# Performance work log

Hardware: AMD Instinct MI355X
Metric: run time of the kernel (lower is better)

## Reference

```python
import math
import jax, jax.numpy as jnp
import numpy as np

B, T, C, H = 1, 2048, 1024, 16


def _rope(q, k):
    # q, k: (B, H, T, D); interleaved RoPE exactly as the torch helper
    D = q.shape[-1]
    pos = jnp.arange(q.shape[2], dtype=jnp.float32)[:, None]           # (T, 1)
    div = jnp.exp(jnp.arange(0, D, 2, dtype=jnp.float32) * (-math.log(10000.0) / D))
    ang = pos * div                                                     # (T, D/2)
    sin = jnp.repeat(jnp.sin(ang), 2, axis=-1)                          # [s0,s0,s1,s1,...]
    cos = jnp.repeat(jnp.cos(ang), 2, axis=-1)

    def rot(x):
        x_alt = jnp.stack([-x[..., 1::2], x[..., ::2]], axis=-1).reshape(x.shape)
        return x * cos + x_alt * sin

    return rot(q), rot(k)


def setup_inputs() -> dict:
    key = jax.random.key(0)
    ks = jax.random.split(key, 5)
    s = 1.0 / math.sqrt(C)
    return {
        "x": jax.random.normal(ks[0], (B, T, C), dtype=jnp.float32),
        "Wq": jax.random.normal(ks[1], (C, C), dtype=jnp.float32) * s,
        "bq": jnp.zeros((C,), dtype=jnp.float32),
        "Wk": jax.random.normal(ks[2], (C, C), dtype=jnp.float32) * s,
        "bk": jnp.zeros((C,), dtype=jnp.float32),
        "Wv": jax.random.normal(ks[3], (C, C), dtype=jnp.float32) * s,
        "bv": jnp.zeros((C,), dtype=jnp.float32),
        "Wp": jax.random.normal(ks[4], (C, C), dtype=jnp.float32) * s,
        "bp": jnp.zeros((C,), dtype=jnp.float32),
    }


def reference(x, Wq, bq, Wk, bk, Wv, bv, Wp, bp):
    b, t, c = x.shape
    d = c // H
    # QKV projections -> (B, H, T, D)
    def split_heads(y):
        return y.reshape(b, t, H, d).transpose(0, 2, 1, 3)

    q = split_heads(x @ Wq + bq)
    k = split_heads(x @ Wk + bk)
    v = split_heads(x @ Wv + bv)
    q, k = _rope(q, k)

    scale = 1.0 / math.sqrt(d)
    att = jnp.einsum("bhqd,bhkd->bhqk", q, k) * scale                   # (B,H,T,T)
    causal = jnp.tril(jnp.ones((t, t), dtype=bool))                     # (T,T)
    att = jnp.where(causal[None, None], att, -jnp.inf)
    att = jax.nn.softmax(att, axis=-1)
    attn_save = att
    # dropout p=0 (eval) -> identity
    y = jnp.einsum("bhqk,bhkd->bhqd", att, v)                           # (B,H,T,D)
    y = y.transpose(0, 2, 1, 3).reshape(b, t, c)
    y = y @ Wp + bp
    return y, attn_save
```

## Files before the change

kernel.cpp:

```cpp
#include <hip/hip_runtime.h>

typedef unsigned short ushort_t;
typedef __bf16 bf16x8 __attribute__((ext_vector_type(8)));
typedef float f32x4 __attribute__((ext_vector_type(4)));

#define T_DIM 2048
#define C_DIM 1024
#define H_NUM 16
#define D_DIM 64

__device__ __forceinline__ ushort_t f2bf(float f){
  unsigned v = __float_as_uint(f);
  return (ushort_t)((v + 0x7fffu + ((v >> 16) & 1u)) >> 16);
}
__device__ __forceinline__ float bf2f(ushort_t u){
  return __uint_as_float(((unsigned)u) << 16);
}

typedef __attribute__((address_space(1))) const unsigned int* gas1_t;
typedef __attribute__((address_space(3))) unsigned int* las3_t;

__device__ __forceinline__ void gload_lds16(const void* g, void* l){
  __builtin_amdgcn_global_load_lds((gas1_t)g, (las3_t)l, 16, 0, 0);
}

__global__ __launch_bounds__(256) void prep_kernel(
    const float* __restrict__ x, ushort_t* __restrict__ xb,
    const float* __restrict__ w0, const float* __restrict__ w1,
    const float* __restrict__ w2, const float* __restrict__ w3,
    ushort_t* __restrict__ t0, ushort_t* __restrict__ t1,
    ushort_t* __restrict__ t2, ushort_t* __restrict__ t3)
{
  __shared__ float tl[64][65];
  const int bid = blockIdx.x;
  const int tid = threadIdx.x;
  if (bid >= 1024){
    int i = ((bid - 1024) * 256 + tid) * 4;
    float4 v = *reinterpret_cast<const float4*>(x + i);
    ushort4 o;
    o.x = f2bf(v.x); o.y = f2bf(v.y); o.z = f2bf(v.z); o.w = f2bf(v.w);
    *reinterpret_cast<ushort4*>(xb + i) = o;
    return;
  }
  const int which = bid >> 8;
  const float* W = which==0 ? w0 : which==1 ? w1 : which==2 ? w2 : w3;
  ushort_t* WT   = which==0 ? t0 : which==1 ? t1 : which==2 ? t2 : t3;
  const int tile = bid & 255;
  const int k0 = (tile & 15) * 64;
  const int n0 = (tile >> 4) * 64;
#pragma unroll
  for (int i = 0; i < 16; ++i){
    int idx = tid + i * 256;
    int r = idx >> 6, c = idx & 63;
    tl[r][c] = W[(k0 + r) * C_DIM + n0 + c];
  }
  __syncthreads();
#pragma unroll
  for (int i = 0; i < 16; ++i){
    int idx = tid + i * 256;
    int r = idx >> 6, c = idx & 63;
    WT[(n0 + r) * C_DIM + k0 + c] = f2bf(tl[c][r]);
  }
}

template<int MODE>
__global__ __launch_bounds__(256) void gemm_kernel(
    const ushort_t* __restrict__ A,
    const ushort_t* __restrict__ bt0, const ushort_t* __restrict__ bt1, const ushort_t* __restrict__ bt2,
    const float* __restrict__ bias0, const float* __restrict__ bias1, const float* __restrict__ bias2,
    ushort_t* __restrict__ o0, ushort_t* __restrict__ o1, ushort_t* __restrict__ o2,
    float* __restrict__ fo)
{
  __shared__ __align__(16) ushort_t Alds[64 * 32];
  __shared__ __align__(16) ushort_t Blds[128 * 32];
  const int tid = threadIdx.x;
  const int l15 = tid & 15, g = (tid & 63) >> 4;
  const int w = tid >> 6, wr = w >> 1, wc = w & 1;
  const int m0 = blockIdx.x * 64;
  int byy = blockIdx.y;
  int sel = 0;
  const ushort_t* BT; const float* bias; ushort_t* outp;
  if (MODE == 0){
    sel = byy >> 3; byy &= 7;
    BT   = sel==0 ? bt0 : (sel==1 ? bt1 : bt2);
    bias = sel==0 ? bias0 : (sel==1 ? bias1 : bias2);
    outp = sel==0 ? o0 : (sel==1 ? o1 : o2);
  } else { BT = bt0; bias = bias0; outp = o0; }
  const int n0 = byy * 128;

  const int c0 = tid, c1 = tid + 256;
  const ushort_t* Asrc  = A + (m0 + (c0 >> 2)) * C_DIM + (c0 & 3) * 8;
  const ushort_t* Bsrc0 = BT + (n0 + (c0 >> 2)) * C_DIM + (c0 & 3) * 8;
  const ushort_t* Bsrc1 = BT + (n0 + (c1 >> 2)) * C_DIM + (c1 & 3) * 8;

  f32x4 acc[2][4] = {};

  for (int kt = 0; kt < 32; ++kt){
    const int ko = kt * 32;
    gload_lds16(Asrc + ko, &Alds[c0 * 8]);
    gload_lds16(Bsrc0 + ko, &Blds[c0 * 8]);
    gload_lds16(Bsrc1 + ko, &Blds[c1 * 8]);
    __syncthreads();
    bf16x8 af[2], bfr[4];
#pragma unroll
    for (int i = 0; i < 2; ++i)
      af[i] = *reinterpret_cast<const bf16x8*>(&Alds[(wr * 32 + i * 16 + l15) * 32 + g * 8]);
#pragma unroll
    for (int j = 0; j < 4; ++j)
      bfr[j] = *reinterpret_cast<const bf16x8*>(&Blds[(wc * 64 + j * 16 + l15) * 32 + g * 8]);
#pragma unroll
    for (int i = 0; i < 2; ++i)
#pragma unroll
      for (int j = 0; j < 4; ++j)
        acc[i][j] = __builtin_amdgcn_mfma_f32_16x16x32_bf16(af[i], bfr[j], acc[i][j], 0, 0, 0);
    __syncthreads();
  }

  float bvv[4];
#pragma unroll
  for (int j = 0; j < 4; ++j) bvv[j] = bias[n0 + wc * 64 + j * 16 + l15];

  if (MODE == 1){
#pragma unroll
    for (int i = 0; i < 2; ++i)
#pragma unroll
      for (int j = 0; j < 4; ++j)
#pragma unroll
        for (int e = 0; e < 4; ++e){
          int t = m0 + wr * 32 + i * 16 + g * 4 + e;
          int c = n0 + wc * 64 + j * 16 + l15;
          fo[t * C_DIM + c] = acc[i][j][e] + bvv[j];
        }
    return;
  }

  if (sel == 2){
#pragma unroll
    for (int i = 0; i < 2; ++i){
#pragma unroll
      for (int j = 0; j < 4; ++j){
        int c = n0 + wc * 64 + j * 16 + l15;
        int hh = c >> 6, d = c & 63;
        int t0e = m0 + wr * 32 + i * 16 + g * 4;
        ushort4 o;
        o.x = f2bf(acc[i][j][0] + bvv[j]);
        o.y = f2bf(acc[i][j][1] + bvv[j]);
        o.z = f2bf(acc[i][j][2] + bvv[j]);
        o.w = f2bf(acc[i][j][3] + bvv[j]);
        *reinterpret_cast<ushort4*>(outp + (size_t)(hh * D_DIM + d) * T_DIM + t0e) = o;
      }
    }
  } else {
#pragma unroll
    for (int i = 0; i < 2; ++i){
#pragma unroll
      for (int j = 0; j < 4; ++j){
#pragma unroll
        for (int e = 0; e < 4; ++e){
          int t = m0 + wr * 32 + i * 16 + g * 4 + e;
          int c = n0 + wc * 64 + j * 16 + l15;
          int hh = c >> 6, d = c & 63;
          outp[((size_t)(hh * T_DIM) + t) * D_DIM + d] = f2bf(acc[i][j][e] + bvv[j]);
        }
      }
    }
  }
}

__global__ void rope_kernel(ushort_t* __restrict__ Qb, ushort_t* __restrict__ Kb){
  int gid = blockIdx.x * 256 + threadIdx.x;
  int which = gid >> 20;
  int r = gid & ((1 << 20) - 1);
  int i = r & 31;
  int t = (r >> 5) & 2047;
  int hh = r >> 16;
  ushort_t* P = which ? Kb : Qb;
  unsigned* p = reinterpret_cast<unsigned*>(P + ((hh * T_DIM) + t) * D_DIM + 2 * i);
  unsigned pv = *p;
  float x0 = bf2f((ushort_t)(pv & 0xffffu));
  float x1 = bf2f((ushort_t)(pv >> 16));
  float ang = (float)t * __expf((float)i * -0.2878231366242558f);
  float sn, cs;
  __sincosf(ang, &sn, &cs);
  float y0 = x0 * cs - x1 * sn;
  float y1 = x1 * cs + x0 * sn;
  *p = (unsigned)f2bf(y0) | (((unsigned)f2bf(y1)) << 16);
}

__global__ __launch_bounds__(256) void attn_kernel(
    const ushort_t* __restrict__ Qb, const ushort_t* __restrict__ Kb,
    const ushort_t* __restrict__ Vt, float* __restrict__ att, ushort_t* __restrict__ ya)
{
  __shared__ __align__(16) ushort_t Plds[2][64 * 72];
  __shared__ float m_sh[64], l_sh[64];

  const int tid = threadIdx.x;
  const int l15 = tid & 15, g = (tid & 63) >> 4;
  const int w = tid >> 6, wr = w >> 1, wc = w & 1;
  const int lin = (int)blockIdx.x;
  const int h = 2 * (lin & 7) + ((lin >> 3) & 1);
  const int qi = (T_DIM / 64 - 1) - (lin >> 4);
  const int q0 = qi * 64;
  const int nkt = qi + 1;

  const ushort_t* Qh = Qb + h * T_DIM * D_DIM;
  const ushort_t* Kh = Kb + h * T_DIM * D_DIM;
  const ushort_t* Vh = Vt + h * D_DIM * T_DIM;
  float* atth = att + (size_t)h * T_DIM * T_DIM;

  const f32x4 fz = {0.f, 0.f, 0.f, 0.f};
  const float scale = 0.125f;

  const int qloc = w * 16 + l15;
  const int qglob = q0 + qloc;
  bf16x8 qT[2];
#pragma unroll
  for (int ks = 0; ks < 2; ++ks)
    qT[ks] = *reinterpret_cast<const bf16x8*>(Qh + qglob * D_DIM + ks * 32 + g * 8);

  float m1 = -1e30f, l1 = 0.f;

  for (int kt = 0; kt < nkt; ++kt){
    f32x4 sc[4];
    sc[0] = fz; sc[1] = fz; sc[2] = fz; sc[3] = fz;
#pragma unroll
    for (int mblk = 0; mblk < 4; ++mblk){
#pragma unroll
      for (int ks = 0; ks < 2; ++ks){
        bf16x8 kfT = *reinterpret_cast<const bf16x8*>(
            Kh + (kt * 64 + mblk * 16 + l15) * D_DIM + ks * 32 + g * 8);
        sc[mblk] = __builtin_amdgcn_mfma_f32_16x16x32_bf16(kfT, qT[ks], sc[mblk], 0, 0, 0);
      }
    }
    const bool diag = (kt == qi);
    const int kbase = kt * 64 + g * 4;
    float sv[16];
    float mx = -1e30f;
#pragma unroll
    for (int mblk = 0; mblk < 4; ++mblk){
#pragma unroll
      for (int j = 0; j < 4; ++j){
        float s = sc[mblk][j] * scale;
        if (diag && (kbase + mblk * 16 + j) > qglob) s = -1e30f;
        sv[mblk * 4 + j] = s;
        mx = fmaxf(mx, s);
      }
    }
    mx = fmaxf(mx, __shfl_xor(mx, 16));
    mx = fmaxf(mx, __shfl_xor(mx, 32));
    float mn = fmaxf(m1, mx);
    float ps = 0.f;
#pragma unroll
    for (int i = 0; i < 16; ++i) ps += __expf(sv[i] - mn);
    ps += __shfl_xor(ps, 16);
    ps += __shfl_xor(ps, 32);
    l1 = l1 * __expf(m1 - mn) + ps;
    m1 = mn;
  }

  if ((tid & 48) == 0){ m_sh[qloc] = m1; l_sh[qloc] = l1; }
  __syncthreads();

  float Mrow[2][4], Li[2][4];
#pragma unroll
  for (int ms = 0; ms < 2; ++ms)
#pragma unroll
    for (int j = 0; j < 4; ++j){
      int row = wr * 32 + ms * 16 + g * 4 + j;
      Mrow[ms][j] = m_sh[row];
      Li[ms][j] = 1.0f / l_sh[row];
    }

  bf16x8 qf[2][2];
#pragma unroll
  for (int ms = 0; ms < 2; ++ms)
#pragma unroll
    for (int ks = 0; ks < 2; ++ks)
      qf[ms][ks] = *reinterpret_cast<const bf16x8*>(
          Qh + (q0 + wr * 32 + ms * 16 + l15) * D_DIM + ks * 32 + g * 8);

  f32x4 yac[2][2];
  yac[0][0] = fz; yac[0][1] = fz; yac[1][0] = fz; yac[1][1] = fz;

  int pb = 0;
  for (int kt = 0; kt < nkt; ++kt){
    ushort_t* Pb = &Plds[pb][0];
    bf16x8 kf[2][2];
#pragma unroll
    for (int ns = 0; ns < 2; ++ns)
#pragma unroll
      for (int ks = 0; ks < 2; ++ks)
        kf[ns][ks] = *reinterpret_cast<const bf16x8*>(
            Kh + (kt * 64 + wc * 32 + ns * 16 + l15) * D_DIM + ks * 32 + g * 8);

    f32x4 sac[2][2];
    sac[0][0] = fz; sac[0][1] = fz; sac[1][0] = fz; sac[1][1] = fz;
#pragma unroll
    for (int ms = 0; ms < 2; ++ms)
#pragma unroll
      for (int ns = 0; ns < 2; ++ns)
#pragma unroll
        for (int ks = 0; ks < 2; ++ks)
          sac[ms][ns] = __builtin_amdgcn_mfma_f32_16x16x32_bf16(qf[ms][ks], kf[ns][ks], sac[ms][ns], 0, 0, 0);

    const bool diag = (kt == qi);
#pragma unroll
    for (int ms = 0; ms < 2; ++ms)
#pragma unroll
      for (int ns = 0; ns < 2; ++ns)
#pragma unroll
        for (int j = 0; j < 4; ++j){
          float s = sac[ms][ns][j] * scale;
          int qq = wr * 32 + ms * 16 + g * 4 + j;
          int cc = wc * 32 + ns * 16 + l15;
          if (diag && cc > qq) s = -1e30f;
          float p = __expf(s - Mrow[ms][j]) * Li[ms][j];
          Pb[qq * 72 + cc] = f2bf(p);
        }
    __syncthreads();

    bf16x8 pf[2][2], vf[2][2];
#pragma unroll
    for (int ms = 0; ms < 2; ++ms)
#pragma unroll
      for (int kk = 0; kk < 2; ++kk)
        pf[ms][kk] = *reinterpret_cast<const bf16x8*>(
            &Pb[(wr * 32 + ms * 16 + l15) * 72 + kk * 32 + g * 8]);
#pragma unroll
    for (int nd = 0; nd < 2; ++nd)
#pragma unroll
      for (int kk = 0; kk < 2; ++kk)
        vf[nd][kk] = *reinterpret_cast<const bf16x8*>(
            Vh + (wc * 32 + nd * 16 + l15) * T_DIM + kt * 64 + kk * 32 + g * 8);
#pragma unroll
    for (int ms = 0; ms < 2; ++ms)
#pragma unroll
      for (int nd = 0; nd < 2; ++nd)
#pragma unroll
        for (int kk = 0; kk < 2; ++kk)
          yac[ms][nd] = __builtin_amdgcn_mfma_f32_16x16x32_bf16(pf[ms][kk], vf[nd][kk], yac[ms][nd], 0, 0, 0);

#pragma unroll
    for (int half = 0; half < 2; ++half){
      const int c = tid + half * 256;
      const int r = c >> 3, s = c & 7;
      union { int4 i4; ushort_t us[8]; } u;
      u.i4 = *reinterpret_cast<const int4*>(&Pb[r * 72 + s * 8]);
      f32x4 lo = { bf2f(u.us[0]), bf2f(u.us[1]), bf2f(u.us[2]), bf2f(u.us[3]) };
      f32x4 hi = { bf2f(u.us[4]), bf2f(u.us[5]), bf2f(u.us[6]), bf2f(u.us[7]) };
      float* dst = atth + (size_t)(q0 + r) * T_DIM + kt * 64 + s * 8;
      __builtin_nontemporal_store(lo, reinterpret_cast<f32x4*>(dst));
      __builtin_nontemporal_store(hi, reinterpret_cast<f32x4*>(dst) + 1);
    }
    pb ^= 1;
  }

  const int zc0 = nkt * 64;
  const int cpr = (T_DIM - zc0) >> 2;
  if (cpr > 0){
    const f32x4 z = {0.f, 0.f, 0.f, 0.f};
    for (int r = 0; r < 64; ++r){
      f32x4* dst = reinterpret_cast<f32x4*>(atth + (size_t)(q0 + r) * T_DIM + zc0);
      for (int i = tid; i < cpr; i += 256)
        __builtin_nontemporal_store(z, dst + i);
    }
  }

#pragma unroll
  for (int ms = 0; ms < 2; ++ms)
#pragma unroll
    for (int nd = 0; nd < 2; ++nd)
#pragma unroll
      for (int j = 0; j < 4; ++j){
        int t = q0 + wr * 32 + ms * 16 + g * 4 + j;
        int dcol = wc * 32 + nd * 16 + l15;
        ya[t * C_DIM + h * D_DIM + dcol] = f2bf(yac[ms][nd][j]);
      }
}

extern "C" void kernel_launch(void* const* d_in, const int* in_sizes, int n_in,
                              void* d_out, int out_size, void* d_ws, size_t ws_size,
                              hipStream_t stream)
{
  const float* x  = (const float*)d_in[0];
  const float* Wq = (const float*)d_in[1];
  const float* bq = (const float*)d_in[2];
  const float* Wk = (const float*)d_in[3];
  const float* bk = (const float*)d_in[4];
  const float* Wv = (const float*)d_in[5];
  const float* bv = (const float*)d_in[6];
  const float* Wp = (const float*)d_in[7];
  const float* bp = (const float*)d_in[8];
  float* out = (float*)d_out;
  char* ws = (char*)d_ws;

  ushort_t* xb  = (ushort_t*)(ws);
  ushort_t* wtq = (ushort_t*)(ws + (4u  << 20));
  ushort_t* wtk = (ushort_t*)(ws + (6u  << 20));
  ushort_t* wtv = (ushort_t*)(ws + (8u  << 20));
  ushort_t* wtp = (ushort_t*)(ws + (10u << 20));
  ushort_t* Qb  = (ushort_t*)(ws + (12u << 20));
  ushort_t* Kb  = (ushort_t*)(ws + (16u << 20));
  ushort_t* Vt  = (ushort_t*)(ws + (20u << 20));
  ushort_t* ya  = (ushort_t*)(ws + (24u << 20));

  hipLaunchKernelGGL(prep_kernel, dim3(3072), dim3(256), 0, stream,
                     x, xb, Wq, Wk, Wv, Wp, wtq, wtk, wtv, wtp);
  hipLaunchKernelGGL((gemm_kernel<0>), dim3(32, 24), dim3(256), 0, stream,
                     xb, wtq, wtk, wtv, bq, bk, bv, Qb, Kb, Vt, nullptr);
  hipLaunchKernelGGL(rope_kernel, dim3(8192), dim3(256), 0, stream, Qb, Kb);
  hipLaunchKernelGGL(attn_kernel, dim3(512), dim3(256), 0, stream,
                     Qb, Kb, Vt, out + 2097152, ya);
  hipLaunchKernelGGL((gemm_kernel<1>), dim3(32, 8), dim3(256), 0, stream,
                     ya, wtp, nullptr, nullptr, bp, nullptr, nullptr,
                     nullptr, nullptr, nullptr, out);
}
```

Measured before the change: 181.1 us.

## Split attention along key tiles into two halves with stats merge and reduction

```diff
diff --git a/kernel.cpp b/kernel.cpp
--- a/kernel.cpp
+++ b/kernel.cpp
@@ -187,21 +187,103 @@
   *p = (unsigned)f2bf(y0) | (((unsigned)f2bf(y1)) << 16);
 }
 
-__global__ __launch_bounds__(256) void attn_kernel(
+__global__ __launch_bounds__(256) void attn_pass1_kernel(
     const ushort_t* __restrict__ Qb, const ushort_t* __restrict__ Kb,
-    const ushort_t* __restrict__ Vt, float* __restrict__ att, ushort_t* __restrict__ ya)
+    float* __restrict__ mS, float* __restrict__ lS)
+{
+  const int tid = threadIdx.x;
+  const int l15 = tid & 15, g = (tid & 63) >> 4;
+  const int w = tid >> 6;
+  const int lin = (int)blockIdx.x;
+  const int h = 2 * (lin & 7) + ((lin >> 3) & 1);
+  const int rest = lin >> 4;
+  const int qi = 31 - (rest >> 1);
+  const int s = rest & 1;
+  const int q0 = qi * 64;
+  const int nkt = qi + 1;
+  const int n1 = (nkt + 1) >> 1;
+  const int kt0 = s ? n1 : 0;
+  const int kt1 = s ? nkt : n1;
+
+  const ushort_t* Qh = Qb + h * T_DIM * D_DIM;
+  const ushort_t* Kh = Kb + h * T_DIM * D_DIM;
+  const f32x4 fz = {0.f, 0.f, 0.f, 0.f};
+  const float scale = 0.125f;
+
+  const int qloc = w * 16 + l15;
+  const int qglob = q0 + qloc;
+  bf16x8 qT[2];
+#pragma unroll
+  for (int ks = 0; ks < 2; ++ks)
+    qT[ks] = *reinterpret_cast<const bf16x8*>(Qh + qglob * D_DIM + ks * 32 + g * 8);
+
+  float m1 = -1e30f, l1 = 0.f;
+
+  for (int kt = kt0; kt < kt1; ++kt){
+    f32x4 sc[4];
+    sc[0] = fz; sc[1] = fz; sc[2] = fz; sc[3] = fz;
+#pragma unroll
+    for (int mblk = 0; mblk < 4; ++mblk){
+#pragma unroll
+      for (int ks = 0; ks < 2; ++ks){
+        bf16x8 kfT = *reinterpret_cast<const bf16x8*>(
+            Kh + (kt * 64 + mblk * 16 + l15) * D_DIM + ks * 32 + g * 8);
+        sc[mblk] = __builtin_amdgcn_mfma_f32_16x16x32_bf16(kfT, qT[ks], sc[mblk], 0, 0, 0);
+      }
+    }
+    const bool diag = (kt == qi);
+    const int kbase = kt * 64 + g * 4;
+    float sv[16];
+    float mx = -1e30f;
+#pragma unroll
+    for (int mblk = 0; mblk < 4; ++mblk){
+#pragma unroll
+      for (int j = 0; j < 4; ++j){
+        float sx = sc[mblk][j] * scale;
+        if (diag && (kbase + mblk * 16 + j) > qglob) sx = -1e30f;
+        sv[mblk * 4 + j] = sx;
+        mx = fmaxf(mx, sx);
+      }
+    }
+    mx = fmaxf(mx, __shfl_xor(mx, 16));
+    mx = fmaxf(mx, __shfl_xor(mx, 32));
+    float mn = fmaxf(m1, mx);
+    float ps = 0.f;
+#pragma unroll
+    for (int i = 0; i < 16; ++i) ps += __expf(sv[i] - mn);
+    ps += __shfl_xor(ps, 16);
+    ps += __shfl_xor(ps, 32);
+    l1 = l1 * __expf(m1 - mn) + ps;
+    m1 = mn;
+  }
+
+  if ((tid & 48) == 0){
+    mS[(h * 2 + s) * T_DIM + qglob] = m1;
+    lS[(h * 2 + s) * T_DIM + qglob] = l1;
+  }
+}
+
+__global__ __launch_bounds__(256) void attn_pass2_kernel(
+    const ushort_t* __restrict__ Qb, const ushort_t* __restrict__ Kb,
+    const ushort_t* __restrict__ Vt,
+    const float* __restrict__ mS, const float* __restrict__ lS,
+    float* __restrict__ att, float* __restrict__ yp)
 {
   __shared__ __align__(16) ushort_t Plds[2][64 * 72];
-  __shared__ float m_sh[64], l_sh[64];
 
   const int tid = threadIdx.x;
   const int l15 = tid & 15, g = (tid & 63) >> 4;
   const int w = tid >> 6, wr = w >> 1, wc = w & 1;
   const int lin = (int)blockIdx.x;
   const int h = 2 * (lin & 7) + ((lin >> 3) & 1);
-  const int qi = (T_DIM / 64 - 1) - (lin >> 4);
+  const int rest = lin >> 4;
+  const int qi = 31 - (rest >> 1);
+  const int s = rest & 1;
   const int q0 = qi * 64;
   const int nkt = qi + 1;
+  const int n1 = (nkt + 1) >> 1;
+  const int kt0 = s ? n1 : 0;
+  const int kt1 = s ? nkt : n1;
 
   const ushort_t* Qh = Qb + h * T_DIM * D_DIM;
   const ushort_t* Kh = Kb + h * T_DIM * D_DIM;
@@ -211,64 +293,20 @@
   const f32x4 fz = {0.f, 0.f, 0.f, 0.f};
   const float scale = 0.125f;
 
-  const int qloc = w * 16 + l15;
-  const int qglob = q0 + qloc;
-  bf16x8 qT[2];
-#pragma unroll
-  for (int ks = 0; ks < 2; ++ks)
-    qT[ks] = *reinterpret_cast<const bf16x8*>(Qh + qglob * D_DIM + ks * 32 + g * 8);
-
-  float m1 = -1e30f, l1 = 0.f;
-
-  for (int kt = 0; kt < nkt; ++kt){
-    f32x4 sc[4];
-    sc[0] = fz; sc[1] = fz; sc[2] = fz; sc[3] = fz;
-#pragma unroll
-    for (int mblk = 0; mblk < 4; ++mblk){
-#pragma unroll
-      for (int ks = 0; ks < 2; ++ks){
-        bf16x8 kfT = *reinterpret_cast<const bf16x8*>(
-            Kh + (kt * 64 + mblk * 16 + l15) * D_DIM + ks * 32 + g * 8);
-        sc[mblk] = __builtin_amdgcn_mfma_f32_16x16x32_bf16(kfT, qT[ks], sc[mblk], 0, 0, 0);
-      }
-    }
-    const bool diag = (kt == qi);
-    const int kbase = kt * 64 + g * 4;
-    float sv[16];
-    float mx = -1e30f;
-#pragma unroll
-    for (int mblk = 0; mblk < 4; ++mblk){
-#pragma unroll
-      for (int j = 0; j < 4; ++j){
-        float s = sc[mblk][j] * scale;
-        if (diag && (kbase + mblk * 16 + j) > qglob) s = -1e30f;
-        sv[mblk * 4 + j] = s;
-        mx = fmaxf(mx, s);
-      }
-    }
-    mx = fmaxf(mx, __shfl_xor(mx, 16));
-    mx = fmaxf(mx, __shfl_xor(mx, 32));
-    float mn = fmaxf(m1, mx);
-    float ps = 0.f;
-#pragma unroll
-    for (int i = 0; i < 16; ++i) ps += __expf(sv[i] - mn);
-    ps += __shfl_xor(ps, 16);
-    ps += __shfl_xor(ps, 32);
-    l1 = l1 * __expf(m1 - mn) + ps;
-    m1 = mn;
-  }
-
-  if ((tid & 48) == 0){ m_sh[qloc] = m1; l_sh[qloc] = l1; }
-  __syncthreads();
-
   float Mrow[2][4], Li[2][4];
 #pragma unroll
   for (int ms = 0; ms < 2; ++ms)
 #pragma unroll
     for (int j = 0; j < 4; ++j){
-      int row = wr * 32 + ms * 16 + g * 4 + j;
-      Mrow[ms][j] = m_sh[row];
-      Li[ms][j] = 1.0f / l_sh[row];
+      int row = q0 + wr * 32 + ms * 16 + g * 4 + j;
+      float ma = mS[(h * 2 + 0) * T_DIM + row];
+      float mb = mS[(h * 2 + 1) * T_DIM + row];
+      float la = lS[(h * 2 + 0) * T_DIM + row];
+      float lb = lS[(h * 2 + 1) * T_DIM + row];
+      float M = fmaxf(ma, mb);
+      float L = la * __expf(ma - M) + lb * __expf(mb - M);
+      Mrow[ms][j] = M;
+      Li[ms][j] = 1.0f / L;
     }
 
   bf16x8 qf[2][2];
@@ -283,7 +321,7 @@
   yac[0][0] = fz; yac[0][1] = fz; yac[1][0] = fz; yac[1][1] = fz;
 
   int pb = 0;
-  for (int kt = 0; kt < nkt; ++kt){
+  for (int kt = kt0; kt < kt1; ++kt){
     ushort_t* Pb = &Plds[pb][0];
     bf16x8 kf[2][2];
 #pragma unroll
@@ -310,11 +348,11 @@
       for (int ns = 0; ns < 2; ++ns)
 #pragma unroll
         for (int j = 0; j < 4; ++j){
-          float s = sac[ms][ns][j] * scale;
+          float sx = sac[ms][ns][j] * scale;
           int qq = wr * 32 + ms * 16 + g * 4 + j;
           int cc = wc * 32 + ns * 16 + l15;
-          if (diag && cc > qq) s = -1e30f;
-          float p = __expf(s - Mrow[ms][j]) * Li[ms][j];
+          if (diag && cc > qq) sx = -1e30f;
+          float p = __expf(sx - Mrow[ms][j]) * Li[ms][j];
           Pb[qq * 72 + cc] = f2bf(p);
         }
     __syncthreads();
@@ -343,29 +381,32 @@
 #pragma unroll
     for (int half = 0; half < 2; ++half){
       const int c = tid + half * 256;
-      const int r = c >> 3, s = c & 7;
+      const int r = c >> 3, sx = c & 7;
       union { int4 i4; ushort_t us[8]; } u;
-      u.i4 = *reinterpret_cast<const int4*>(&Pb[r * 72 + s * 8]);
+      u.i4 = *reinterpret_cast<const int4*>(&Pb[r * 72 + sx * 8]);
       f32x4 lo = { bf2f(u.us[0]), bf2f(u.us[1]), bf2f(u.us[2]), bf2f(u.us[3]) };
       f32x4 hi = { bf2f(u.us[4]), bf2f(u.us[5]), bf2f(u.us[6]), bf2f(u.us[7]) };
-      float* dst = atth + (size_t)(q0 + r) * T_DIM + kt * 64 + s * 8;
+      float* dst = atth + (size_t)(q0 + r) * T_DIM + kt * 64 + sx * 8;
       __builtin_nontemporal_store(lo, reinterpret_cast<f32x4*>(dst));
       __builtin_nontemporal_store(hi, reinterpret_cast<f32x4*>(dst) + 1);
     }
     pb ^= 1;
   }
 
-  const int zc0 = nkt * 64;
-  const int cpr = (T_DIM - zc0) >> 2;
-  if (cpr > 0){
-    const f32x4 z = {0.f, 0.f, 0.f, 0.f};
-    for (int r = 0; r < 64; ++r){
-      f32x4* dst = reinterpret_cast<f32x4*>(atth + (size_t)(q0 + r) * T_DIM + zc0);
-      for (int i = tid; i < cpr; i += 256)
-        __builtin_nontemporal_store(z, dst + i);
-    }
-  }
-
+  if (s == 1){
+    const int zc0 = nkt * 64;
+    const int cpr = (T_DIM - zc0) >> 2;
+    if (cpr > 0){
+      const f32x4 z = {0.f, 0.f, 0.f, 0.f};
+      for (int r = 0; r < 64; ++r){
+        f32x4* dst = reinterpret_cast<f32x4*>(atth + (size_t)(q0 + r) * T_DIM + zc0);
+        for (int i = tid; i < cpr; i += 256)
+          __builtin_nontemporal_store(z, dst + i);
+      }
+    }
+  }
+
+  float* ypd = yp + (size_t)s * (T_DIM * C_DIM);
 #pragma unroll
   for (int ms = 0; ms < 2; ++ms)
 #pragma unroll
@@ -374,8 +415,21 @@
       for (int j = 0; j < 4; ++j){
         int t = q0 + wr * 32 + ms * 16 + g * 4 + j;
         int dcol = wc * 32 + nd * 16 + l15;
-        ya[t * C_DIM + h * D_DIM + dcol] = f2bf(yac[ms][nd][j]);
-      }
+        ypd[(size_t)t * C_DIM + h * D_DIM + dcol] = yac[ms][nd][j];
+      }
+}
+
+__global__ void y_reduce_kernel(const float* __restrict__ yp, ushort_t* __restrict__ ya)
+{
+  int i = (blockIdx.x * 256 + threadIdx.x) * 4;
+  float4 a = *reinterpret_cast<const float4*>(yp + i);
+  float4 b = *reinterpret_cast<const float4*>(yp + (T_DIM * C_DIM) + i);
+  ushort4 o;
+  o.x = f2bf(a.x + b.x);
+  o.y = f2bf(a.y + b.y);
+  o.z = f2bf(a.z + b.z);
+  o.w = f2bf(a.w + b.w);
+  *reinterpret_cast<ushort4*>(ya + i) = o;
 }
 
 extern "C" void kernel_launch(void* const* d_in, const int* in_sizes, int n_in,
@@ -403,14 +457,20 @@
   ushort_t* Kb  = (ushort_t*)(ws + (16u << 20));
   ushort_t* Vt  = (ushort_t*)(ws + (20u << 20));
   ushort_t* ya  = (ushort_t*)(ws + (24u << 20));
+  float*    mS  = (float*)   (ws + (28u << 20));
+  float*    lS  = (float*)   (ws + (28u << 20) + (256u << 10));
+  float*    yp  = (float*)   (ws + (29u << 20));
 
   hipLaunchKernelGGL(prep_kernel, dim3(3072), dim3(256), 0, stream,
                      x, xb, Wq, Wk, Wv, Wp, wtq, wtk, wtv, wtp);
   hipLaunchKernelGGL((gemm_kernel<0>), dim3(32, 24), dim3(256), 0, stream,
                      xb, wtq, wtk, wtv, bq, bk, bv, Qb, Kb, Vt, nullptr);
   hipLaunchKernelGGL(rope_kernel, dim3(8192), dim3(256), 0, stream, Qb, Kb);
-  hipLaunchKernelGGL(attn_kernel, dim3(512), dim3(256), 0, stream,
-                     Qb, Kb, Vt, out + 2097152, ya);
+  hipLaunchKernelGGL(attn_pass1_kernel, dim3(1024), dim3(256), 0, stream,
+                     Qb, Kb, mS, lS);
+  hipLaunchKernelGGL(attn_pass2_kernel, dim3(1024), dim3(256), 0, stream,
+                     Qb, Kb, Vt, mS, lS, out + 2097152, yp);
+  hipLaunchKernelGGL(y_reduce_kernel, dim3(2048), dim3(256), 0, stream, yp, ya);
   hipLaunchKernelGGL((gemm_kernel<1>), dim3(32, 8), dim3(256), 0, stream,
                      ya, wtp, nullptr, nullptr, bp, nullptr, nullptr,
                      nullptr, nullptr, nullptr, out);
```

Result: slower. 220.1 us (+21.6%).

## Halve attention query block to 32 rows and split stats pass across key halves

Applied to the files above, without the earlier changes.

```diff
diff --git a/kernel.cpp b/kernel.cpp
--- a/kernel.cpp
+++ b/kernel.cpp
@@ -8,6 +8,7 @@
 #define C_DIM 1024
 #define H_NUM 16
 #define D_DIM 64
+#define QBLK 32
 
 __device__ __forceinline__ ushort_t f2bf(float f){
   unsigned v = __float_as_uint(f);
@@ -191,17 +192,19 @@
     const ushort_t* __restrict__ Qb, const ushort_t* __restrict__ Kb,
     const ushort_t* __restrict__ Vt, float* __restrict__ att, ushort_t* __restrict__ ya)
 {
-  __shared__ __align__(16) ushort_t Plds[2][64 * 72];
-  __shared__ float m_sh[64], l_sh[64];
+  __shared__ __align__(16) ushort_t Plds[2][QBLK * 72];
+  __shared__ float m_sh[2][QBLK], l_sh[2][QBLK];
 
   const int tid = threadIdx.x;
   const int l15 = tid & 15, g = (tid & 63) >> 4;
-  const int w = tid >> 6, wr = w >> 1, wc = w & 1;
+  const int w = tid >> 6;
   const int lin = (int)blockIdx.x;
   const int h = 2 * (lin & 7) + ((lin >> 3) & 1);
-  const int qi = (T_DIM / 64 - 1) - (lin >> 4);
-  const int q0 = qi * 64;
-  const int nkt = qi + 1;
+  const int qi = 63 - (lin >> 4);
+  const int q0 = qi * QBLK;
+  const int nkt = (qi >> 1) + 1;
+  const int kd = nkt - 1;
+  const int qoff = (qi & 1) * 32;
 
   const ushort_t* Qh = Qb + h * T_DIM * D_DIM;
   const ushort_t* Kh = Kb + h * T_DIM * D_DIM;
@@ -211,8 +214,9 @@
   const f32x4 fz = {0.f, 0.f, 0.f, 0.f};
   const float scale = 0.125f;
 
-  const int qloc = w * 16 + l15;
-  const int qglob = q0 + qloc;
+  const int qsel = w & 1, khalf = w >> 1;
+  const int lq = qsel * 16 + l15;
+  const int qglob = q0 + lq;
   bf16x8 qT[2];
 #pragma unroll
   for (int ks = 0; ks < 2; ++ks)
@@ -220,7 +224,7 @@
 
   float m1 = -1e30f, l1 = 0.f;
 
-  for (int kt = 0; kt < nkt; ++kt){
+  for (int kt = khalf; kt < nkt; kt += 2){
     f32x4 sc[4];
     sc[0] = fz; sc[1] = fz; sc[2] = fz; sc[3] = fz;
 #pragma unroll
@@ -232,8 +236,7 @@
         sc[mblk] = __builtin_amdgcn_mfma_f32_16x16x32_bf16(kfT, qT[ks], sc[mblk], 0, 0, 0);
       }
     }
-    const bool diag = (kt == qi);
-    const int kbase = kt * 64 + g * 4;
+    const bool diag = (kt == kd);
     float sv[16];
     float mx = -1e30f;
 #pragma unroll
@@ -241,7 +244,7 @@
 #pragma unroll
       for (int j = 0; j < 4; ++j){
         float s = sc[mblk][j] * scale;
-        if (diag && (kbase + mblk * 16 + j) > qglob) s = -1e30f;
+        if (diag && (mblk * 16 + g * 4 + j) > (qoff + lq)) s = -1e30f;
         sv[mblk * 4 + j] = s;
         mx = fmaxf(mx, s);
       }
@@ -258,29 +261,29 @@
     m1 = mn;
   }
 
-  if ((tid & 48) == 0){ m_sh[qloc] = m1; l_sh[qloc] = l1; }
+  if (g == 0){ m_sh[khalf][lq] = m1; l_sh[khalf][lq] = l1; }
   __syncthreads();
 
-  float Mrow[2][4], Li[2][4];
-#pragma unroll
-  for (int ms = 0; ms < 2; ++ms)
-#pragma unroll
-    for (int j = 0; j < 4; ++j){
-      int row = wr * 32 + ms * 16 + g * 4 + j;
-      Mrow[ms][j] = m_sh[row];
-      Li[ms][j] = 1.0f / l_sh[row];
-    }
-
-  bf16x8 qf[2][2];
-#pragma unroll
-  for (int ms = 0; ms < 2; ++ms)
-#pragma unroll
-    for (int ks = 0; ks < 2; ++ks)
-      qf[ms][ks] = *reinterpret_cast<const bf16x8*>(
-          Qh + (q0 + wr * 32 + ms * 16 + l15) * D_DIM + ks * 32 + g * 8);
-
-  f32x4 yac[2][2];
-  yac[0][0] = fz; yac[0][1] = fz; yac[1][0] = fz; yac[1][1] = fz;
+  const int wr = w >> 1, wc = w & 1;
+  float Mrow[4], Li[4];
+#pragma unroll
+  for (int j = 0; j < 4; ++j){
+    int row = wr * 16 + g * 4 + j;
+    float ma = m_sh[0][row], mb = m_sh[1][row];
+    float M = fmaxf(ma, mb);
+    float L = l_sh[0][row] * __expf(ma - M) + l_sh[1][row] * __expf(mb - M);
+    Mrow[j] = M;
+    Li[j] = 1.0f / L;
+  }
+
+  bf16x8 qf[2];
+#pragma unroll
+  for (int ks = 0; ks < 2; ++ks)
+    qf[ks] = *reinterpret_cast<const bf16x8*>(
+        Qh + (q0 + wr * 16 + l15) * D_DIM + ks * 32 + g * 8);
+
+  f32x4 yac[2];
+  yac[0] = fz; yac[1] = fz;
 
   int pb = 0;
   for (int kt = 0; kt < nkt; ++kt){
@@ -293,39 +296,33 @@
         kf[ns][ks] = *reinterpret_cast<const bf16x8*>(
             Kh + (kt * 64 + wc * 32 + ns * 16 + l15) * D_DIM + ks * 32 + g * 8);
 
-    f32x4 sac[2][2];
-    sac[0][0] = fz; sac[0][1] = fz; sac[1][0] = fz; sac[1][1] = fz;
-#pragma unroll
-    for (int ms = 0; ms < 2; ++ms)
-#pragma unroll
-      for (int ns = 0; ns < 2; ++ns)
-#pragma unroll
-        for (int ks = 0; ks < 2; ++ks)
-          sac[ms][ns] = __builtin_amdgcn_mfma_f32_16x16x32_bf16(qf[ms][ks], kf[ns][ks], sac[ms][ns], 0, 0, 0);
-
-    const bool diag = (kt == qi);
-#pragma unroll
-    for (int ms = 0; ms < 2; ++ms)
-#pragma unroll
-      for (int ns = 0; ns < 2; ++ns)
-#pragma unroll
-        for (int j = 0; j < 4; ++j){
-          float s = sac[ms][ns][j] * scale;
-          int qq = wr * 32 + ms * 16 + g * 4 + j;
-          int cc = wc * 32 + ns * 16 + l15;
-          if (diag && cc > qq) s = -1e30f;
-          float p = __expf(s - Mrow[ms][j]) * Li[ms][j];
-          Pb[qq * 72 + cc] = f2bf(p);
-        }
+    f32x4 sac[2];
+    sac[0] = fz; sac[1] = fz;
+#pragma unroll
+    for (int ns = 0; ns < 2; ++ns)
+#pragma unroll
+      for (int ks = 0; ks < 2; ++ks)
+        sac[ns] = __builtin_amdgcn_mfma_f32_16x16x32_bf16(qf[ks], kf[ns][ks], sac[ns], 0, 0, 0);
+
+    const bool diag = (kt == kd);
+#pragma unroll
+    for (int ns = 0; ns < 2; ++ns)
+#pragma unroll
+      for (int j = 0; j < 4; ++j){
+        float s = sac[ns][j] * scale;
+        int qq = wr * 16 + g * 4 + j;
+        int cc = wc * 32 + ns * 16 + l15;
+        if (diag && cc > (qoff + qq)) s = -1e30f;
+        float p = __expf(s - Mrow[j]) * Li[j];
+        Pb[qq * 72 + cc] = f2bf(p);
+      }
     __syncthreads();
 
-    bf16x8 pf[2][2], vf[2][2];
-#pragma unroll
-    for (int ms = 0; ms < 2; ++ms)
-#pragma unroll
-      for (int kk = 0; kk < 2; ++kk)
-        pf[ms][kk] = *reinterpret_cast<const bf16x8*>(
-            &Pb[(wr * 32 + ms * 16 + l15) * 72 + kk * 32 + g * 8]);
+    bf16x8 pf[2], vf[2][2];
+#pragma unroll
+    for (int kk = 0; kk < 2; ++kk)
+      pf[kk] = *reinterpret_cast<const bf16x8*>(
+          &Pb[(wr * 16 + l15) * 72 + kk * 32 + g * 8]);
 #pragma unroll
     for (int nd = 0; nd < 2; ++nd)
 #pragma unroll
@@ -333,17 +330,13 @@
         vf[nd][kk] = *reinterpret_cast<const bf16x8*>(
             Vh + (wc * 32 + nd * 16 + l15) * T_DIM + kt * 64 + kk * 32 + g * 8);
 #pragma unroll
-    for (int ms = 0; ms < 2; ++ms)
-#pragma unroll
-      for (int nd = 0; nd < 2; ++nd)
-#pragma unroll
-        for (int kk = 0; kk < 2; ++kk)
-          yac[ms][nd] = __builtin_amdgcn_mfma_f32_16x16x32_bf16(pf[ms][kk], vf[nd][kk], yac[ms][nd], 0, 0, 0);
-
-#pragma unroll
-    for (int half = 0; half < 2; ++half){
-      const int c = tid + half * 256;
-      const int r = c >> 3, s = c & 7;
+    for (int nd = 0; nd < 2; ++nd)
+#pragma unroll
+      for (int kk = 0; kk < 2; ++kk)
+        yac[nd] = __builtin_amdgcn_mfma_f32_16x16x32_bf16(pf[kk], vf[nd][kk], yac[nd], 0, 0, 0);
+
+    {
+      const int r = tid >> 3, s = tid & 7;
       union { int4 i4; ushort_t us[8]; } u;
       u.i4 = *reinterpret_cast<const int4*>(&Pb[r * 72 + s * 8]);
       f32x4 lo = { bf2f(u.us[0]), bf2f(u.us[1]), bf2f(u.us[2]), bf2f(u.us[3]) };
@@ -359,7 +352,7 @@
   const int cpr = (T_DIM - zc0) >> 2;
   if (cpr > 0){
     const f32x4 z = {0.f, 0.f, 0.f, 0.f};
-    for (int r = 0; r < 64; ++r){
+    for (int r = 0; r < QBLK; ++r){
       f32x4* dst = reinterpret_cast<f32x4*>(atth + (size_t)(q0 + r) * T_DIM + zc0);
       for (int i = tid; i < cpr; i += 256)
         __builtin_nontemporal_store(z, dst + i);
@@ -367,15 +360,13 @@
   }
 
 #pragma unroll
-  for (int ms = 0; ms < 2; ++ms)
-#pragma unroll
-    for (int nd = 0; nd < 2; ++nd)
-#pragma unroll
-      for (int j = 0; j < 4; ++j){
-        int t = q0 + wr * 32 + ms * 16 + g * 4 + j;
-        int dcol = wc * 32 + nd * 16 + l15;
-        ya[t * C_DIM + h * D_DIM + dcol] = f2bf(yac[ms][nd][j]);
-      }
+  for (int nd = 0; nd < 2; ++nd)
+#pragma unroll
+    for (int j = 0; j < 4; ++j){
+      int t = q0 + wr * 16 + g * 4 + j;
+      int dcol = wc * 32 + nd * 16 + l15;
+      ya[t * C_DIM + h * D_DIM + dcol] = f2bf(yac[nd][j]);
+    }
 }
 
 extern "C" void kernel_launch(void* const* d_in, const int* in_sizes, int n_in,
@@ -409,7 +400,7 @@
   hipLaunchKernelGGL((gemm_kernel<0>), dim3(32, 24), dim3(256), 0, stream,
                      xb, wtq, wtk, wtv, bq, bk, bv, Qb, Kb, Vt, nullptr);
   hipLaunchKernelGGL(rope_kernel, dim3(8192), dim3(256), 0, stream, Qb, Kb);
-  hipLaunchKernelGGL(attn_kernel, dim3(512), dim3(256), 0, stream,
+  hipLaunchKernelGGL(attn_kernel, dim3(1024), dim3(256), 0, stream,
                      Qb, Kb, Vt, out + 2097152, ya);
   hipLaunchKernelGGL((gemm_kernel<1>), dim3(32, 8), dim3(256), 0, stream,
                      ya, wtp, nullptr, nullptr, bp, nullptr, nullptr,
```

Result: slower. 208.7 us (+15.2%).
